# Optimization experiments

Measured on AMD Instinct MI355X. Metric: run time of the kernel, lower is better.

Reference implementation:

```python
import jax, jax.numpy as jnp
import numpy as np
import math

B, N, H = 32, 512, 512  # batch, nodes_num (=input_dim), hidden_dim; upscale=1.0 -> d_qk = H


def setup_inputs() -> dict:
    key = jax.random.key(0)
    ks = jax.random.split(key, 4)
    s = 1.0 / math.sqrt(H)
    x = jax.random.normal(ks[0], (B, N, H), dtype=jnp.float32)
    Wq = jax.random.normal(ks[1], (H, H), dtype=jnp.float32) * s
    Wk = jax.random.normal(ks[2], (H, H), dtype=jnp.float32) * s
    Wm = jax.random.normal(ks[3], (N * H, H), dtype=jnp.float32) * (1.0 / math.sqrt(N * H))
    return {
        "x": x,
        "Wq": Wq, "bq": jnp.zeros((H,), jnp.float32),
        "Wk": Wk, "bk": jnp.zeros((H,), jnp.float32),
        "Wm": Wm, "bm": jnp.zeros((H,), jnp.float32),
    }


def reference(x, Wq, bq, Wk, bk, Wm, bm):
    # q/k projections (Linear stored as (in, out))
    q = jnp.einsum('bnh,hd->bnd', x, Wq) + bq          # [B,N,D]
    k = jnp.einsum('bnh,hd->bnd', x, Wk) + bk          # [B,N,D]
    d = q.shape[-1]
    scores = jnp.einsum('bnd,bmd->bnm', q, k) / math.sqrt(d)
    attention = jax.nn.softmax(jax.nn.sigmoid(scores), axis=-1)  # [B,N,N]
    out = jnp.einsum('bnm,bmh->bnh', attention, x)     # dropout = identity (eval)
    b, n, h = x.shape
    out = out.reshape(b, n * h) @ Wm + bm              # [B,H]
    return (out, attention)
```

## Files before the change

kernel.cpp:

```cpp
#include <hip/hip_runtime.h>

#define BB 32
#define NN 512
#define HH 512
constexpr float QK_SCALE = 0.04419417382415922f;

using bf16x8 = __attribute__((ext_vector_type(8))) short;
using f32x4  = __attribute__((ext_vector_type(4))) float;

__device__ __forceinline__ short f2bf(float f) {
  unsigned int u = __float_as_uint(f);
  unsigned int r = (u + 0x7FFFu + ((u >> 16) & 1u)) >> 16;
  return (short)r;
}

__global__ __launch_bounds__(256) void prep_x(const float* __restrict__ x,
                                              short* __restrict__ xbf,
                                              short* __restrict__ xT) {
  __shared__ float tile[32][33];
  const int b = blockIdx.z;
  const int n0 = blockIdx.y * 32, h0 = blockIdx.x * 32;
  const int t = threadIdx.x;
  const int i = t >> 3;
  const int j4 = (t & 7) * 4;
  const float4 v = *(const float4*)&x[((long)b * NN + n0 + i) * HH + h0 + j4];
  short o[4] = {f2bf(v.x), f2bf(v.y), f2bf(v.z), f2bf(v.w)};
  *(uint2*)&xbf[((long)b * NN + n0 + i) * HH + h0 + j4] = *(uint2*)o;
  tile[i][j4 + 0] = v.x; tile[i][j4 + 1] = v.y;
  tile[i][j4 + 2] = v.z; tile[i][j4 + 3] = v.w;
  __syncthreads();
  short p[4] = {f2bf(tile[j4 + 0][i]), f2bf(tile[j4 + 1][i]),
                f2bf(tile[j4 + 2][i]), f2bf(tile[j4 + 3][i])};
  *(uint2*)&xT[((long)b * HH + h0 + i) * NN + n0 + j4] = *(uint2*)p;
}

__global__ __launch_bounds__(256) void prep_w(const float* __restrict__ Wq,
                                              const float* __restrict__ Wk,
                                              short* __restrict__ Wqt,
                                              short* __restrict__ Wkt) {
  __shared__ float tile[32][33];
  const float* W = blockIdx.z ? Wk : Wq;
  short* Wt = blockIdx.z ? Wkt : Wqt;
  const int h0 = blockIdx.y * 32, d0 = blockIdx.x * 32;
  const int t = threadIdx.x;
  const int i = t >> 3;
  const int j4 = (t & 7) * 4;
  const float4 v = *(const float4*)&W[(long)(h0 + i) * HH + d0 + j4];
  tile[i][j4 + 0] = v.x; tile[i][j4 + 1] = v.y;
  tile[i][j4 + 2] = v.z; tile[i][j4 + 3] = v.w;
  __syncthreads();
  short p[4] = {f2bf(tile[j4 + 0][i]), f2bf(tile[j4 + 1][i]),
                f2bf(tile[j4 + 2][i]), f2bf(tile[j4 + 3][i])};
  *(uint2*)&Wt[(long)(d0 + i) * HH + h0 + j4] = *(uint2*)p;
}

template <int WRITE_BF16>
__global__ __launch_bounds__(256) void gemm_bt(const short* __restrict__ A,
                                               const short* __restrict__ Bt,
                                               void* __restrict__ Cv,
                                               const float* __restrict__ bias,
                                               float scale, int M, int Nc, int K,
                                               long sA, long sB, long sC) {
  __shared__ short As[64][72];
  __shared__ short Bs[64][72];
  A += (long)blockIdx.z * sA;
  Bt += (long)blockIdx.z * sB;
  const int m0 = blockIdx.x * 64;
  const int n0 = blockIdx.y * 64;
  const int t = threadIdx.x;
  const int wave = t >> 6, lane = t & 63;
  const int lrow = lane & 15, lq = lane >> 4;
  const int srow = t >> 2;
  const int scol = (t & 3) * 16;
  f32x4 acc[4] = {};
  const short* Ar = A + (long)(m0 + srow) * K + scol;
  const short* Br = Bt + (long)(n0 + srow) * K + scol;
  for (int k0 = 0; k0 < K; k0 += 64) {
    *(uint4*)&As[srow][scol]     = *(const uint4*)&Ar[k0];
    *(uint4*)&As[srow][scol + 8] = *(const uint4*)&Ar[k0 + 8];
    *(uint4*)&Bs[srow][scol]     = *(const uint4*)&Br[k0];
    *(uint4*)&Bs[srow][scol + 8] = *(const uint4*)&Br[k0 + 8];
    __syncthreads();
#pragma unroll
    for (int kk = 0; kk < 64; kk += 32) {
      bf16x8 a = *(bf16x8*)&As[wave * 16 + lrow][kk + lq * 8];
#pragma unroll
      for (int nt = 0; nt < 4; ++nt) {
        bf16x8 b = *(bf16x8*)&Bs[nt * 16 + lrow][kk + lq * 8];
        acc[nt] = __builtin_amdgcn_mfma_f32_16x16x32_bf16(a, b, acc[nt], 0, 0, 0);
      }
    }
    __syncthreads();
  }
  const long cbase = (long)blockIdx.z * sC;
#pragma unroll
  for (int nt = 0; nt < 4; ++nt) {
#pragma unroll
    for (int r = 0; r < 4; ++r) {
      const int row = m0 + wave * 16 + lq * 4 + r;
      const int col = n0 + nt * 16 + lrow;
      float v = acc[nt][r] * scale;
      if (bias) v += bias[col];
      if (WRITE_BF16)
        ((short*)Cv)[cbase + (long)row * Nc + col] = f2bf(v);
      else
        ((float*)Cv)[cbase + (long)row * Nc + col] = v;
    }
  }
}

__global__ __launch_bounds__(256) void sigsoftmax(float* __restrict__ att,
                                                  short* __restrict__ attbf) {
  const long row = blockIdx.x;
  float* p = att + row * NN;
  const int t = threadIdx.x;
  float2 v = *(float2*)&p[t * 2];
  const float s0 = 1.f / (1.f + __expf(-v.x));
  const float s1 = 1.f / (1.f + __expf(-v.y));
  const float e0 = __expf(s0), e1 = __expf(s1);
  float sum = e0 + e1;
#pragma unroll
  for (int o = 32; o > 0; o >>= 1) sum += __shfl_down(sum, o);
  __shared__ float wsum[4];
  if ((t & 63) == 0) wsum[t >> 6] = sum;
  __syncthreads();
  const float r = 1.f / (wsum[0] + wsum[1] + wsum[2] + wsum[3]);
  const float a0 = e0 * r, a1 = e1 * r;
  float2 o2; o2.x = a0; o2.y = a1;
  *(float2*)&p[t * 2] = o2;
  short pk[2] = {f2bf(a0), f2bf(a1)};
  *(unsigned int*)&attbf[row * NN + t * 2] = *(unsigned int*)pk;
}

__global__ __launch_bounds__(256) void init_out(float* __restrict__ out,
                                                const float* __restrict__ bm) {
  const int t = blockIdx.x * 256 + threadIdx.x;
  out[t] = bm[t & (HH - 1)];
}

__global__ __launch_bounds__(256) void gemm_final(const short* __restrict__ A,
                                                  const float* __restrict__ Wm,
                                                  float* __restrict__ out) {
  __shared__ short As[32][40];
  __shared__ short Bs[64][40];
  const int j0 = blockIdx.y * 64;
  const long KT = (long)NN * HH;
  const long Kc = KT / gridDim.x;
  const long i0base = (long)blockIdx.x * Kc;
  const int t = threadIdx.x;
  const int wave = t >> 6, lane = t & 63;
  const int lrow = lane & 15, lq = lane >> 4;
  const int jj = t & 63;
  const int rb = (t >> 6) * 8;
  f32x4 acc[2] = {};
  for (long i0 = i0base; i0 < i0base + Kc; i0 += 32) {
    if (t < 128) {
      const int ar = t >> 2;
      const int ac = (t & 3) * 8;
      *(uint4*)&As[ar][ac] = *(const uint4*)&A[(long)ar * KT + i0 + ac];
    }
#pragma unroll
    for (int r = 0; r < 8; ++r) {
      Bs[jj][rb + r] = f2bf(Wm[(i0 + rb + r) * HH + j0 + jj]);
    }
    __syncthreads();
    bf16x8 b  = *(bf16x8*)&Bs[wave * 16 + lrow][lq * 8];
    bf16x8 a0 = *(bf16x8*)&As[lrow][lq * 8];
    bf16x8 a1 = *(bf16x8*)&As[16 + lrow][lq * 8];
    acc[0] = __builtin_amdgcn_mfma_f32_16x16x32_bf16(a0, b, acc[0], 0, 0, 0);
    acc[1] = __builtin_amdgcn_mfma_f32_16x16x32_bf16(a1, b, acc[1], 0, 0, 0);
    __syncthreads();
  }
#pragma unroll
  for (int mt = 0; mt < 2; ++mt)
#pragma unroll
    for (int r = 0; r < 4; ++r) {
      const int brow = mt * 16 + lq * 4 + r;
      const int col = j0 + wave * 16 + lrow;
      atomicAdd(&out[(long)brow * HH + col], acc[mt][r]);
    }
}

extern "C" void kernel_launch(void* const* d_in, const int* in_sizes, int n_in,
                              void* d_out, int out_size, void* d_ws, size_t ws_size,
                              hipStream_t stream) {
  const float* x  = (const float*)d_in[0];
  const float* Wq = (const float*)d_in[1];
  const float* bq = (const float*)d_in[2];
  const float* Wk = (const float*)d_in[3];
  const float* bk = (const float*)d_in[4];
  const float* Wm = (const float*)d_in[5];
  const float* bm = (const float*)d_in[6];
  float* out = (float*)d_out;
  float* att = out + (long)BB * HH;

  char* ws = (char*)d_ws;
  const long SZ = (long)BB * NN * HH * sizeof(short);
  short* buf0 = (short*)ws;
  short* buf1 = (short*)(ws + SZ);
  short* buf2 = (short*)(ws + 2 * SZ);
  short* buf3 = (short*)(ws + 3 * SZ);
  short* wqt  = (short*)(ws + 4 * SZ);
  short* wkt  = wqt + (long)HH * HH;

  prep_x<<<dim3(HH / 32, NN / 32, BB), 256, 0, stream>>>(x, buf0, buf1);
  prep_w<<<dim3(HH / 32, HH / 32, 2), 256, 0, stream>>>(Wq, Wk, wqt, wkt);

  gemm_bt<1><<<dim3(BB * NN / 64, HH / 64, 1), 256, 0, stream>>>(
      buf0, wqt, buf2, bq, 1.f, BB * NN, HH, HH, 0, 0, 0);
  gemm_bt<1><<<dim3(BB * NN / 64, HH / 64, 1), 256, 0, stream>>>(
      buf0, wkt, buf3, bk, 1.f, BB * NN, HH, HH, 0, 0, 0);

  gemm_bt<0><<<dim3(NN / 64, NN / 64, BB), 256, 0, stream>>>(
      buf2, buf3, att, nullptr, QK_SCALE, NN, NN, HH,
      (long)NN * HH, (long)NN * HH, (long)NN * NN);

  sigsoftmax<<<dim3(BB * NN), 256, 0, stream>>>(att, buf2);

  gemm_bt<1><<<dim3(NN / 64, HH / 64, BB), 256, 0, stream>>>(
      buf2, buf1, buf0, nullptr, 1.f, NN, HH, NN,
      (long)NN * NN, (long)HH * NN, (long)NN * HH);

  init_out<<<dim3(BB * HH / 256), 256, 0, stream>>>(out, bm);
  gemm_final<<<dim3(256, HH / 64, 1), 256, 0, stream>>>(buf0, Wm, out);
}
```

Measured before the change: 834.2 us.

## Use 128x128 MFMA GEMM tiles with direct global-to-LDS loads and split-K partial reduction

Replaces the 64x64 batched GEMM with a 128x128 tile kernel in which each wave computes a 64x64 sub-tile, and loads operands straight into LDS with global_load_lds. This raises data reuse per load and cuts register-staging overhead. The final Wm GEMM now reads Wm with vectorized float4 loads over a 64-wide K step and writes per-block partial sums to a workspace, replacing atomicAdd into the output. A separate reduce kernel then sums the 128 partials and adds the bias. The unpadded LDS layout may cause bank conflicts, and the larger tiles put fewer blocks on the grid.

```diff
diff --git a/kernel.cpp b/kernel.cpp
--- a/kernel.cpp
+++ b/kernel.cpp
@@ -7,11 +7,18 @@
 
 using bf16x8 = __attribute__((ext_vector_type(8))) short;
 using f32x4  = __attribute__((ext_vector_type(4))) float;
+typedef unsigned int u32;
 
 __device__ __forceinline__ short f2bf(float f) {
   unsigned int u = __float_as_uint(f);
   unsigned int r = (u + 0x7FFFu + ((u >> 16) & 1u)) >> 16;
   return (short)r;
+}
+
+__device__ __forceinline__ void gl_lds16(const short* g, short* l) {
+  __builtin_amdgcn_global_load_lds(
+      (const __attribute__((address_space(1))) u32*)g,
+      (__attribute__((address_space(3))) u32*)l, 16, 0, 0);
 }
 
 __global__ __launch_bounds__(256) void prep_x(const float* __restrict__ x,
@@ -55,56 +62,72 @@
 }
 
 template <int WRITE_BF16>
-__global__ __launch_bounds__(256) void gemm_bt(const short* __restrict__ A,
+__global__ __launch_bounds__(256) void gemm128(const short* __restrict__ A,
                                                const short* __restrict__ Bt,
                                                void* __restrict__ Cv,
                                                const float* __restrict__ bias,
                                                float scale, int M, int Nc, int K,
                                                long sA, long sB, long sC) {
-  __shared__ short As[64][72];
-  __shared__ short Bs[64][72];
-  A += (long)blockIdx.z * sA;
+  __shared__ short As[128 * 64];
+  __shared__ short Bs[128 * 64];
+  A  += (long)blockIdx.z * sA;
   Bt += (long)blockIdx.z * sB;
-  const int m0 = blockIdx.x * 64;
-  const int n0 = blockIdx.y * 64;
+  const int m0 = blockIdx.x * 128;
+  const int n0 = blockIdx.y * 128;
   const int t = threadIdx.x;
   const int wave = t >> 6, lane = t & 63;
   const int lrow = lane & 15, lq = lane >> 4;
-  const int srow = t >> 2;
-  const int scol = (t & 3) * 16;
-  f32x4 acc[4] = {};
-  const short* Ar = A + (long)(m0 + srow) * K + scol;
-  const short* Br = Bt + (long)(n0 + srow) * K + scol;
+  const int wr = (wave >> 1) * 64, wc = (wave & 1) * 64;
+
+  const int srow = t >> 3;
+  const int scol = (t & 7) * 8;
+  const short* Ag = A  + (long)(m0 + srow) * K + scol;
+  const short* Bg = Bt + (long)(n0 + srow) * K + scol;
+  short* Al = &As[srow * 64 + scol];
+  short* Bl = &Bs[srow * 64 + scol];
+  const long gstep = (long)32 * K;
+
+  f32x4 acc[4][4] = {};
   for (int k0 = 0; k0 < K; k0 += 64) {
-    *(uint4*)&As[srow][scol]     = *(const uint4*)&Ar[k0];
-    *(uint4*)&As[srow][scol + 8] = *(const uint4*)&Ar[k0 + 8];
-    *(uint4*)&Bs[srow][scol]     = *(const uint4*)&Br[k0];
-    *(uint4*)&Bs[srow][scol + 8] = *(const uint4*)&Br[k0 + 8];
+#pragma unroll
+    for (int p = 0; p < 4; ++p) {
+      gl_lds16(Ag + k0 + p * gstep, Al + p * 32 * 64);
+      gl_lds16(Bg + k0 + p * gstep, Bl + p * 32 * 64);
+    }
     __syncthreads();
 #pragma unroll
     for (int kk = 0; kk < 64; kk += 32) {
-      bf16x8 a = *(bf16x8*)&As[wave * 16 + lrow][kk + lq * 8];
-#pragma unroll
-      for (int nt = 0; nt < 4; ++nt) {
-        bf16x8 b = *(bf16x8*)&Bs[nt * 16 + lrow][kk + lq * 8];
-        acc[nt] = __builtin_amdgcn_mfma_f32_16x16x32_bf16(a, b, acc[nt], 0, 0, 0);
+      bf16x8 a[4], b[4];
+#pragma unroll
+      for (int i = 0; i < 4; ++i) {
+        a[i] = *(const bf16x8*)&As[(wr + i * 16 + lrow) * 64 + kk + lq * 8];
+        b[i] = *(const bf16x8*)&Bs[(wc + i * 16 + lrow) * 64 + kk + lq * 8];
       }
-    }
-    __syncthreads();
-  }
-  const long cbase = (long)blockIdx.z * sC;
-#pragma unroll
-  for (int nt = 0; nt < 4; ++nt) {
+#pragma unroll
+      for (int m = 0; m < 4; ++m)
+#pragma unroll
+        for (int n = 0; n < 4; ++n)
+          acc[m][n] = __builtin_amdgcn_mfma_f32_16x16x32_bf16(a[m], b[n], acc[m][n], 0, 0, 0);
+    }
+    __syncthreads();
+  }
+
+  const long cb = (long)blockIdx.z * sC;
+#pragma unroll
+  for (int m = 0; m < 4; ++m) {
 #pragma unroll
     for (int r = 0; r < 4; ++r) {
-      const int row = m0 + wave * 16 + lq * 4 + r;
-      const int col = n0 + nt * 16 + lrow;
-      float v = acc[nt][r] * scale;
-      if (bias) v += bias[col];
-      if (WRITE_BF16)
-        ((short*)Cv)[cbase + (long)row * Nc + col] = f2bf(v);
-      else
-        ((float*)Cv)[cbase + (long)row * Nc + col] = v;
+      const long row = m0 + wr + m * 16 + lq * 4 + r;
+#pragma unroll
+      for (int n = 0; n < 4; ++n) {
+        const int col = n0 + wc + n * 16 + lrow;
+        float v = acc[m][n][r] * scale;
+        if (bias) v += bias[col];
+        if (WRITE_BF16)
+          ((short*)Cv)[cb + row * Nc + col] = f2bf(v);
+        else
+          ((float*)Cv)[cb + row * Nc + col] = v;
+      }
     }
   }
 }
@@ -132,53 +155,66 @@
   *(unsigned int*)&attbf[row * NN + t * 2] = *(unsigned int*)pk;
 }
 
-__global__ __launch_bounds__(256) void init_out(float* __restrict__ out,
-                                                const float* __restrict__ bm) {
-  const int t = blockIdx.x * 256 + threadIdx.x;
-  out[t] = bm[t & (HH - 1)];
-}
-
 __global__ __launch_bounds__(256) void gemm_final(const short* __restrict__ A,
                                                   const float* __restrict__ Wm,
-                                                  float* __restrict__ out) {
-  __shared__ short As[32][40];
-  __shared__ short Bs[64][40];
+                                                  float* __restrict__ part) {
+  __shared__ short As[32 * 72];
+  __shared__ short Bs[64 * 72];
   const int j0 = blockIdx.y * 64;
   const long KT = (long)NN * HH;
   const long Kc = KT / gridDim.x;
-  const long i0base = (long)blockIdx.x * Kc;
+  const long i0b = (long)blockIdx.x * Kc;
   const int t = threadIdx.x;
   const int wave = t >> 6, lane = t & 63;
   const int lrow = lane & 15, lq = lane >> 4;
-  const int jj = t & 63;
-  const int rb = (t >> 6) * 8;
+  const int ar = t >> 3, ac = (t & 7) * 8;
+  const int kr = t >> 4, jc = (t & 15) * 4;
   f32x4 acc[2] = {};
-  for (long i0 = i0base; i0 < i0base + Kc; i0 += 32) {
-    if (t < 128) {
-      const int ar = t >> 2;
-      const int ac = (t & 3) * 8;
-      *(uint4*)&As[ar][ac] = *(const uint4*)&A[(long)ar * KT + i0 + ac];
-    }
-#pragma unroll
-    for (int r = 0; r < 8; ++r) {
-      Bs[jj][rb + r] = f2bf(Wm[(i0 + rb + r) * HH + j0 + jj]);
-    }
-    __syncthreads();
-    bf16x8 b  = *(bf16x8*)&Bs[wave * 16 + lrow][lq * 8];
-    bf16x8 a0 = *(bf16x8*)&As[lrow][lq * 8];
-    bf16x8 a1 = *(bf16x8*)&As[16 + lrow][lq * 8];
-    acc[0] = __builtin_amdgcn_mfma_f32_16x16x32_bf16(a0, b, acc[0], 0, 0, 0);
-    acc[1] = __builtin_amdgcn_mfma_f32_16x16x32_bf16(a1, b, acc[1], 0, 0, 0);
-    __syncthreads();
-  }
+  for (long i0 = i0b; i0 < i0b + Kc; i0 += 64) {
+    *(uint4*)&As[ar * 72 + ac] = *(const uint4*)&A[(long)ar * KT + i0 + ac];
+#pragma unroll
+    for (int p = 0; p < 4; ++p) {
+      const float4 w = *(const float4*)&Wm[(i0 + kr + p * 16) * HH + j0 + jc];
+      Bs[(jc + 0) * 72 + kr + p * 16] = f2bf(w.x);
+      Bs[(jc + 1) * 72 + kr + p * 16] = f2bf(w.y);
+      Bs[(jc + 2) * 72 + kr + p * 16] = f2bf(w.z);
+      Bs[(jc + 3) * 72 + kr + p * 16] = f2bf(w.w);
+    }
+    __syncthreads();
+#pragma unroll
+    for (int kk = 0; kk < 64; kk += 32) {
+      bf16x8 b  = *(const bf16x8*)&Bs[(wave * 16 + lrow) * 72 + kk + lq * 8];
+      bf16x8 a0 = *(const bf16x8*)&As[lrow * 72 + kk + lq * 8];
+      bf16x8 a1 = *(const bf16x8*)&As[(16 + lrow) * 72 + kk + lq * 8];
+      acc[0] = __builtin_amdgcn_mfma_f32_16x16x32_bf16(a0, b, acc[0], 0, 0, 0);
+      acc[1] = __builtin_amdgcn_mfma_f32_16x16x32_bf16(a1, b, acc[1], 0, 0, 0);
+    }
+    __syncthreads();
+  }
+  float* dst = part + (long)blockIdx.x * (BB * HH);
 #pragma unroll
   for (int mt = 0; mt < 2; ++mt)
 #pragma unroll
     for (int r = 0; r < 4; ++r) {
-      const int brow = mt * 16 + lq * 4 + r;
+      const int row = mt * 16 + lq * 4 + r;
       const int col = j0 + wave * 16 + lrow;
-      atomicAdd(&out[(long)brow * HH + col], acc[mt][r]);
-    }
+      dst[(long)row * HH + col] = acc[mt][r];
+    }
+}
+
+__global__ __launch_bounds__(256) void reduce_out(const float* __restrict__ part,
+                                                  const float* __restrict__ bm,
+                                                  float* __restrict__ out) {
+  const int idx = blockIdx.x * 256 + threadIdx.x;
+  float s0 = bm[idx & (HH - 1)], s1 = 0.f, s2 = 0.f, s3 = 0.f;
+#pragma unroll 8
+  for (int p = 0; p < 128; p += 4) {
+    s0 += part[(long)(p + 0) * (BB * HH) + idx];
+    s1 += part[(long)(p + 1) * (BB * HH) + idx];
+    s2 += part[(long)(p + 2) * (BB * HH) + idx];
+    s3 += part[(long)(p + 3) * (BB * HH) + idx];
+  }
+  out[idx] = (s0 + s1) + (s2 + s3);
 }
 
 extern "C" void kernel_launch(void* const* d_in, const int* in_sizes, int n_in,
@@ -202,25 +238,26 @@
   short* buf3 = (short*)(ws + 3 * SZ);
   short* wqt  = (short*)(ws + 4 * SZ);
   short* wkt  = wqt + (long)HH * HH;
+  float* part = (float*)buf3;
 
   prep_x<<<dim3(HH / 32, NN / 32, BB), 256, 0, stream>>>(x, buf0, buf1);
   prep_w<<<dim3(HH / 32, HH / 32, 2), 256, 0, stream>>>(Wq, Wk, wqt, wkt);
 
-  gemm_bt<1><<<dim3(BB * NN / 64, HH / 64, 1), 256, 0, stream>>>(
+  gemm128<1><<<dim3(BB * NN / 128, HH / 128, 1), 256, 0, stream>>>(
       buf0, wqt, buf2, bq, 1.f, BB * NN, HH, HH, 0, 0, 0);
-  gemm_bt<1><<<dim3(BB * NN / 64, HH / 64, 1), 256, 0, stream>>>(
+  gemm128<1><<<dim3(BB * NN / 128, HH / 128, 1), 256, 0, stream>>>(
       buf0, wkt, buf3, bk, 1.f, BB * NN, HH, HH, 0, 0, 0);
 
-  gemm_bt<0><<<dim3(NN / 64, NN / 64, BB), 256, 0, stream>>>(
+  gemm128<0><<<dim3(NN / 128, NN / 128, BB), 256, 0, stream>>>(
       buf2, buf3, att, nullptr, QK_SCALE, NN, NN, HH,
       (long)NN * HH, (long)NN * HH, (long)NN * NN);
 
   sigsoftmax<<<dim3(BB * NN), 256, 0, stream>>>(att, buf2);
 
-  gemm_bt<1><<<dim3(NN / 64, HH / 64, BB), 256, 0, stream>>>(
+  gemm128<1><<<dim3(NN / 128, HH / 128, BB), 256, 0, stream>>>(
       buf2, buf1, buf0, nullptr, 1.f, NN, HH, NN,
       (long)NN * NN, (long)HH * NN, (long)NN * HH);
 
-  init_out<<<dim3(BB * HH / 256), 256, 0, stream>>>(out, bm);
-  gemm_final<<<dim3(256, HH / 64, 1), 256, 0, stream>>>(buf0, Wm, out);
-}
+  gemm_final<<<dim3(128, HH / 64, 1), 256, 0, stream>>>(buf0, Wm, part);
+  reduce_out<<<dim3(BB * HH / 256), 256, 0, stream>>>(part, bm, out);
+}
```

Measured after the change: 841.4 us. No clear change (+0.9%).
